# Kernel optimization log

Hardware: AMD Instinct MI355X
Metric: run time of the kernel (lower is better)

## Reference

```python
import jax, jax.numpy as jnp
import numpy as np

NEG_SLOPE = 0.2   # LeakyReLU default negative slope (GATv2 + nn.LeakyReLU)
K_NEIGH = 16      # att_args['num_neighs']


def leaky(x):
    return jnp.where(x >= 0, x, NEG_SLOPE * x)


def knn_idx(x_feat, y_feat, k):
    """Per-batch KNN of y in x (feature space). x_feat,y_feat: [B,M,C] -> [B,M,k] local idx into x."""
    d = (jnp.sum(y_feat * y_feat, -1, keepdims=True)
         - 2.0 * jnp.einsum('bmc,bnc->bmn', y_feat, x_feat)
         + jnp.sum(x_feat * x_feat, -1)[:, None, :])   # [B,M,M]
    _, idx = jax.lax.top_k(-d, k)
    return idx


def gatv2_bipartite(x_last, x_past, nbr, Wl, Wr, att_w):
    """Faithful GATv2Conv((last, past), edge_index) with flow='target_to_source',
    heads H, concat=False (mean over heads), bias=False, no self loops.
    x_j = lin_l(x[0]=last) gathered at knn neighbor (col) indices,
    x_i = lin_r(x[1]=past) at query (row) indices; each query has exactly K edges."""
    N, C = x_last.shape
    H = att_w.shape[0]
    xl = (x_last @ Wl).reshape(N, H, C)          # [N,H,C]
    xr = (x_past @ Wr).reshape(N, H, C)          # [N,H,C]
    xlj = xl[nbr]                                 # [N,K,H,C] gathered source msgs
    e = jnp.einsum('nkhc,hc->nkh', leaky(xlj + xr[:, None]), att_w)  # [N,K,H]
    a = jax.nn.softmax(e, axis=1)                 # softmax over each target's K edges
    out = jnp.einsum('nkh,nkhc->nhc', a, xlj)     # [N,H,C]
    return out.mean(axis=1)                       # concat=False -> head mean, [N,C]


def reference(pc_encoded_seq, W1, b1, W2, b2, Wl, Wr, att_w, batch_size, m_points):
    T, N, C = pc_encoded_seq.shape
    B, M = batch_size, m_points
    G = W2.shape[1]
    # node_level_proj (Linear-LeakyReLU-Linear-LeakyReLU) + global_mean_pool per frame
    h = leaky(leaky(pc_encoded_seq @ W1 + b1) @ W2 + b2)      # [T,N,G]
    global_fea = h.reshape(T, B, M, G).mean(axis=2)            # [T,B,G]
    # frame-level ScaledDotProductAttention: q = last frame, k=v = past frames
    q = global_fea[-1][:, None, :]                             # [B,1,G]
    kv = jnp.transpose(global_fea[:-1], (1, 0, 2))             # [B,T-1,G]
    score = jnp.einsum('bqg,btg->bqt', q, kv) / jnp.sqrt(jnp.asarray(G, jnp.float32))
    attn = jax.nn.softmax(score, axis=-1)                      # [B,1,T-1]
    last = pc_encoded_seq[-1]                                  # [N,C]
    lastb = last.reshape(B, M, C)
    offs = (jnp.arange(B) * M)[:, None, None]
    res = []
    for i in range(T - 1):   # small fixed frame count
        past = pc_encoded_seq[i]
        nbr = knn_idx(past.reshape(B, M, C), lastb, K_NEIGH) + offs  # global idx
        out = gatv2_bipartite(last, past, nbr.reshape(N, K_NEIGH), Wl, Wr, att_w)
        res.append(out.reshape(B, M, C))
    res = jnp.stack(res, axis=1)                               # [B,T-1,M,C]
    fw = attn[:, 0, :, None, None]                             # [B,T-1,1,1]
    weighted = jnp.sum(res * fw, axis=1)                       # [B,M,C]
    tm_out = jnp.concatenate([last, weighted.reshape(N, C)], axis=-1)  # [N,2C]
    return tm_out


def setup_inputs() -> dict:
    key = jax.random.key(0)
    ks = jax.random.split(key, 8)
    T, B, M, C, G, H = 5, 4, 4096, 128, 1024, 4
    N = B * M
    s = lambda fan: 1.0 / np.sqrt(fan)
    return {
        'pc_encoded_seq': jax.random.normal(ks[0], (T, N, C), jnp.float32),
        'W1': jax.random.normal(ks[1], (C, 128), jnp.float32) * s(C),
        'b1': jnp.zeros((128,), jnp.float32),
        'W2': jax.random.normal(ks[2], (128, G), jnp.float32) * s(128),
        'b2': jnp.zeros((G,), jnp.float32),
        'Wl': jax.random.normal(ks[3], (C, H * C), jnp.float32) * s(C),
        'Wr': jax.random.normal(ks[4], (C, H * C), jnp.float32) * s(C),
        'att_w': jax.random.normal(ks[5], (H, C), jnp.float32) * s(C),
        'batch_size': B,
        'm_points': M,
    }
```

## Files before the change

kernel.cpp:

```cpp
#include <hip/hip_runtime.h>
#include <hip/hip_bf16.h>
#include <hip/hip_fp16.h>


typedef __bf16 v8bf __attribute__((ext_vector_type(8)));
typedef float  v4f  __attribute__((ext_vector_type(4)));

__device__ __forceinline__ float lrelu(float x) { return fmaxf(x, 0.2f * x); }

__device__ __forceinline__ unsigned short f2bf(float x) {
  __hip_bfloat16 h = __float2bfloat16(x);
  return __builtin_bit_cast(unsigned short, h);
}
__device__ __forceinline__ float bf2f(unsigned short u) {
  unsigned int t = ((unsigned int)u) << 16;
  return __builtin_bit_cast(float, t);
}

#define GLOAD_LDS16(gp, lp)                                                   \
  __builtin_amdgcn_global_load_lds(                                           \
      (const __attribute__((address_space(1))) void*)(gp),                    \
      (__attribute__((address_space(3))) void*)(lp), 16, 0, 0)

#define RBAR() do { __builtin_amdgcn_s_barrier(); asm volatile("" ::: "memory"); } while (0)
#define LBAR() do { asm volatile("s_waitcnt lgkmcnt(0)" ::: "memory");         \
                    __builtin_amdgcn_s_barrier();                              \
                    asm volatile("" ::: "memory"); } while (0)

template<int EP>
__global__ __launch_bounds__(256, 2)
void nt_mfma(const unsigned short* __restrict__ A, const unsigned short* __restrict__ B,
             const float* __restrict__ aux, void* __restrict__ outv, int K, int ldc)
{
  __shared__ __align__(16) unsigned short smem[3 * 8192];
  const int tid = threadIdx.x;
  const int l = tid & 63;
  const int w = tid >> 6;
  const int wm = w & 1, wn = w >> 1;
  const int m0 = blockIdx.y << 7, n0 = blockIdx.x << 7;
  const int fr = l & 15, quad = l >> 4;
  const int kt = K >> 5;
  const int xq4 = quad ^ ((fr >> 1) & 3);

  const int r0 = tid >> 2;
  const int sw = (tid & 3) ^ ((tid >> 3) & 3);
  const unsigned short* Aa = A + (size_t)(m0 + r0) * K + sw * 8;
  const unsigned short* Ab = Aa + (size_t)64 * K;
  const unsigned short* Ba = B + (size_t)(n0 + r0) * K + sw * 8;
  const unsigned short* Bb = Ba + (size_t)64 * K;

  auto stage = [&](int bi, int ks) {
    unsigned short* As = smem + bi * 8192;
    unsigned short* Bs = As + 4096;
    GLOAD_LDS16(Aa + ks * 32, As + tid * 8);
    GLOAD_LDS16(Ab + ks * 32, As + (tid + 256) * 8);
    GLOAD_LDS16(Ba + ks * 32, Bs + tid * 8);
    GLOAD_LDS16(Bb + ks * 32, Bs + (tid + 256) * 8);
  };

  v4f acc[4][4];
#pragma unroll
  for (int i = 0; i < 4; ++i)
#pragma unroll
    for (int j = 0; j < 4; ++j) acc[i][j] = (v4f){0.f, 0.f, 0.f, 0.f};

  stage(0, 0);
  if (kt > 1) stage(1, 1);
  int cur = 0, pend = (kt > 1) ? 2 : 1, sn = 2;

  for (int ks = 0; ks < kt; ++ks) {
    if (pend == 2) asm volatile("s_waitcnt vmcnt(4)" ::: "memory");
    else           asm volatile("s_waitcnt vmcnt(0)" ::: "memory");
    RBAR();
    int nb = cur + 2; if (nb >= 3) nb -= 3;
    if (sn < kt) { stage(nb, sn); ++sn; } else { --pend; }
    const unsigned short* As = smem + cur * 8192;
    const unsigned short* Bs = As + 4096;
    v8bf af[4], bfr[4];
#pragma unroll
    for (int i = 0; i < 4; ++i)
      af[i] = *(const v8bf*)(As + (wm * 64 + i * 16 + fr) * 32 + xq4 * 8);
#pragma unroll
    for (int j = 0; j < 4; ++j)
      bfr[j] = *(const v8bf*)(Bs + (wn * 64 + j * 16 + fr) * 32 + xq4 * 8);
#pragma unroll
    for (int i = 0; i < 4; ++i)
#pragma unroll
      for (int j = 0; j < 4; ++j)
        acc[i][j] = __builtin_amdgcn_mfma_f32_16x16x32_bf16(af[i], bfr[j], acc[i][j], 0, 0, 0);
    __builtin_amdgcn_sched_barrier(0);
    if (++cur == 3) cur = 0;
  }

  if (EP == 1) {
    unsigned short* O = (unsigned short*)outv;
#pragma unroll
    for (int j = 0; j < 4; ++j) {
      int col = n0 + wn * 64 + j * 16 + fr;
      float bias = aux[col];
#pragma unroll
      for (int i = 0; i < 4; ++i) {
        int row = m0 + wm * 64 + i * 16 + quad * 4;
#pragma unroll
        for (int r = 0; r < 4; ++r)
          O[(size_t)(row + r) * ldc + col] = f2bf(lrelu(acc[i][j][r] + bias));
      }
    }
  } else if (EP == 2) {
    __syncthreads();
    float* red = (float*)smem;
#pragma unroll
    for (int j = 0; j < 4; ++j) {
      int lcol = wn * 64 + j * 16 + fr;
      float bias = aux[n0 + lcol];
      float s = 0.f;
#pragma unroll
      for (int i = 0; i < 4; ++i)
#pragma unroll
        for (int r = 0; r < 4; ++r) s += lrelu(acc[i][j][r] + bias);
      s += __shfl_xor(s, 16);
      s += __shfl_xor(s, 32);
      if (quad == 0) red[w * 128 + lcol] = s;
    }
    __syncthreads();
    if (tid < 128) {
      float s = (tid < 64) ? red[0 * 128 + tid] + red[1 * 128 + tid]
                           : red[2 * 128 + tid] + red[3 * 128 + tid];
      atomicAdd((float*)outv + ((m0 >> 12) << 10) + n0 + tid, s * (1.0f / 4096.0f));
    }
  } else {
    __half* O = (__half*)outv;
#pragma unroll
    for (int j = 0; j < 4; ++j) {
      int col = n0 + wn * 64 + j * 16 + fr;
#pragma unroll
      for (int i = 0; i < 4; ++i) {
        int row = m0 + wm * 64 + i * 16 + quad * 4;
#pragma unroll
        for (int r = 0; r < 4; ++r)
          O[(size_t)(row + r) * ldc + col] = __float2half(acc[i][j][r]);
      }
    }
  }
}

__global__ __launch_bounds__(256, 2)
void knn_fused(const unsigned short* __restrict__ ylay,
               const unsigned short* __restrict__ xlay,
               const float* __restrict__ xsq, int* __restrict__ nbrOut)
{
  __shared__ __align__(16) unsigned short smem[3 * 8192];
  __shared__ float candV[128 * 24];
  __shared__ int   candI[128 * 24];
  __shared__ float tauS[128];
  __shared__ int   cntS[128];
  __shared__ int   flagS;

  const int tid = threadIdx.x;
  const int l = tid & 63;
  const int w = tid >> 6;
  const int wm = w & 1, wn = w >> 1;
  const int pair = blockIdx.x >> 5;
  const int rb = blockIdx.x & 31;
  const int f = pair >> 2, b = pair & 3;
  const int m0 = rb << 7;
  const int fr = l & 15, quad = l >> 4;
  const int xq4 = quad ^ ((fr >> 1) & 3);

  const unsigned short* A = ylay + (size_t)b * 4096 * 384;
  const unsigned short* B = xlay + ((size_t)f * 16384 + (size_t)b * 4096) * 384;
  const float* xq = xsq + f * 16384 + b * 4096;

  const int r0 = tid >> 2;
  const int sw = (tid & 3) ^ ((tid >> 3) & 3);
  const unsigned short* Aa = A + (size_t)(m0 + r0) * 384 + sw * 8;
  const unsigned short* Ab = Aa + 64 * 384;
  const unsigned short* Brow = B + (size_t)r0 * 384 + sw * 8;

  auto stage = [&](int bi, int ct, int ks) {
    unsigned short* As = smem + bi * 8192;
    unsigned short* Bs = As + 4096;
    const unsigned short* Bt = Brow + ct * 49152 + ks * 32;
    GLOAD_LDS16(Aa + ks * 32, As + tid * 8);
    GLOAD_LDS16(Ab + ks * 32, As + (tid + 256) * 8);
    GLOAD_LDS16(Bt, Bs + tid * 8);
    GLOAD_LDS16(Bt + 64 * 384, Bs + (tid + 256) * 8);
  };

  float tv[16];
  int   ti[16];
#pragma unroll
  for (int k = 0; k < 16; ++k) { tv[k] = -3.0e38f; ti[k] = k; }
  float ownMin = -3.0e38f;
  int ownMinPos = 0;
  if (tid < 128) { tauS[tid] = -3.0e38f; cntS[tid] = 0; }
  if (tid == 0) flagS = 0;

  float tc[16];
#pragma unroll
  for (int i = 0; i < 16; ++i) tc[i] = -3.0e38f;

  stage(0, 0, 0);
  stage(1, 0, 1);
  int cur = 0, pend = 2, sct = 0, sks = 2;

  LBAR();

  for (int ct = 0; ct < 32; ++ct) {
    const int n0 = ct << 7;
    float xs[4];
#pragma unroll
    for (int j = 0; j < 4; ++j) xs[j] = xq[n0 + wn * 64 + j * 16 + fr];

    v4f acc[4][4];
#pragma unroll
    for (int i = 0; i < 4; ++i)
#pragma unroll
      for (int j = 0; j < 4; ++j) acc[i][j] = (v4f){0.f, 0.f, 0.f, 0.f};

    for (int ks = 0; ks < 12; ++ks) {
      if (pend == 2) asm volatile("s_waitcnt vmcnt(4)" ::: "memory");
      else           asm volatile("s_waitcnt vmcnt(0)" ::: "memory");
      RBAR();
      int nb = cur + 2; if (nb >= 3) nb -= 3;
      if (sct < 32) {
        stage(nb, sct, sks);
        if (++sks == 12) { sks = 0; ++sct; }
      } else { --pend; }
      const unsigned short* As = smem + cur * 8192;
      const unsigned short* Bs = As + 4096;
      v8bf af[4], bfr[4];
#pragma unroll
      for (int i = 0; i < 4; ++i)
        af[i] = *(const v8bf*)(As + (wm * 64 + i * 16 + fr) * 32 + xq4 * 8);
#pragma unroll
      for (int j = 0; j < 4; ++j)
        bfr[j] = *(const v8bf*)(Bs + (wn * 64 + j * 16 + fr) * 32 + xq4 * 8);
#pragma unroll
      for (int i = 0; i < 4; ++i)
#pragma unroll
        for (int j = 0; j < 4; ++j)
          acc[i][j] = __builtin_amdgcn_mfma_f32_16x16x32_bf16(af[i], bfr[j], acc[i][j], 0, 0, 0);
      __builtin_amdgcn_sched_barrier(0);
      if (++cur == 3) cur = 0;
    }

    unsigned long long pushed = 0ull;
    for (;;) {
#pragma unroll
      for (int i = 0; i < 4; ++i)
#pragma unroll
        for (int r = 0; r < 4; ++r) {
          const int lrow = wm * 64 + i * 16 + quad * 4 + r;
          const float tau = tc[i * 4 + r];
#pragma unroll
          for (int j = 0; j < 4; ++j) {
            const int bit = i * 16 + j * 4 + r;
            float v = 2.f * acc[i][j][r] - xs[j];
            if (v > tau && !((pushed >> bit) & 1ull)) {
              int pos = atomicAdd(&cntS[lrow], 1);
              if (pos < 24) {
                candV[lrow * 24 + pos] = v;
                candI[lrow * 24 + pos] = n0 + wn * 64 + j * 16 + fr;
                pushed |= (1ull << bit);
              }
            }
          }
        }
      LBAR();
      if (tid < 128) {
        int c = cntS[tid];
        int cc = c < 24 ? c : 24;
        for (int q = 0; q < cc; ++q) {
          float v = candV[tid * 24 + q];
          if (v > ownMin) {
            tv[ownMinPos] = v;
            ti[ownMinPos] = candI[tid * 24 + q];
            ownMin = tv[0]; ownMinPos = 0;
#pragma unroll
            for (int k = 1; k < 16; ++k)
              if (tv[k] < ownMin) { ownMin = tv[k]; ownMinPos = k; }
          }
        }
        tauS[tid] = ownMin;
        if (c > 24) flagS = 1;
        cntS[tid] = 0;
      }
      LBAR();
#pragma unroll
      for (int i = 0; i < 4; ++i)
#pragma unroll
        for (int r = 0; r < 4; ++r)
          tc[i * 4 + r] = tauS[wm * 64 + i * 16 + quad * 4 + r];
      int ov = flagS;
      LBAR();
      if (tid == 0) flagS = 0;
      if (!ov) break;
    }
  }

  if (tid < 128) {
    const int base = b * 4096;
    int* outp = nbrOut + ((size_t)(f * 16384 + b * 4096) + m0 + tid) * 16;
#pragma unroll
    for (int k = 0; k < 16; ++k) outp[k] = base + ti[k];
  }
}

__global__ __launch_bounds__(256)
void convert_inputs(const float* __restrict__ seq, unsigned short* __restrict__ seqbf,
                    unsigned short* __restrict__ ylay, unsigned short* __restrict__ xlay,
                    float* __restrict__ xsq)
{
  const int tid = threadIdx.x;
  const int row = blockIdx.x * 8 + (tid >> 5);
  const int c4 = tid & 31;
  float4 v = *(const float4*)(seq + (size_t)row * 128 + c4 * 4);
  ushort4 hi, lo;
  hi.x = f2bf(v.x); lo.x = f2bf(v.x - bf2f(hi.x));
  hi.y = f2bf(v.y); lo.y = f2bf(v.y - bf2f(hi.y));
  hi.z = f2bf(v.z); lo.z = f2bf(v.z - bf2f(hi.z));
  hi.w = f2bf(v.w); lo.w = f2bf(v.w - bf2f(hi.w));
  *(ushort4*)(seqbf + (size_t)row * 128 + c4 * 4) = hi;
  float ss = v.x * v.x + v.y * v.y + v.z * v.z + v.w * v.w;
#pragma unroll
  for (int off = 16; off; off >>= 1) ss += __shfl_xor(ss, off);
  if (row < 65536) {
    unsigned short* p = xlay + (size_t)row * 384 + c4 * 4;
    *(ushort4*)(p) = hi; *(ushort4*)(p + 128) = lo; *(ushort4*)(p + 256) = hi;
    if (c4 == 0) xsq[row] = ss;
  } else {
    unsigned short* p = ylay + (size_t)(row - 65536) * 384 + c4 * 4;
    *(ushort4*)(p) = hi; *(ushort4*)(p + 128) = hi; *(ushort4*)(p + 256) = lo;
  }
}

__global__ __launch_bounds__(256)
void convert_weights(const float* __restrict__ W1, const float* __restrict__ W2,
                     const float* __restrict__ Wl, const float* __restrict__ Wr,
                     const float* __restrict__ aw,
                     unsigned short* __restrict__ W1t, unsigned short* __restrict__ W2t,
                     unsigned short* __restrict__ Wlv, unsigned short* __restrict__ Wrv,
                     __half* __restrict__ awh)
{
  int idx = blockIdx.x * 256 + threadIdx.x;
  if (idx < 16384) {
    int n = idx >> 7, k = idx & 127;
    W1t[idx] = f2bf(W1[k * 128 + n]);
  } else if (idx < 147456) {
    int i = idx - 16384; int n = i >> 7, k = i & 127;
    W2t[i] = f2bf(W2[k * 1024 + n]);
  } else if (idx < 344064) {
    int i = idx - 147456; int n = i / 384, k = i % 384;
    int s = k >> 7, kk = k & 127;
    float wv = Wl[kk * 512 + n];
    unsigned short h = f2bf(wv);
    Wlv[i] = (s == 1) ? f2bf(wv - bf2f(h)) : h;
  } else if (idx < 540672) {
    int i = idx - 344064; int n = i / 384, k = i % 384;
    int s = k >> 7, kk = k & 127;
    float wv = Wr[kk * 512 + n];
    unsigned short h = f2bf(wv);
    Wrv[i] = (s == 2) ? f2bf(wv - bf2f(h)) : h;
  } else if (idx < 541184) {
    int i = idx - 540672;
    awh[i] = __float2half(aw[i]);
  }
}

__global__ __launch_bounds__(1024)
void temporal_attn(const float* __restrict__ gfea, float* __restrict__ attnw)
{
  const int tid = threadIdx.x;
  const int w = tid >> 6, l = tid & 63;
  const int b = w >> 2, i = w & 3;
  const float* q  = gfea + (16 + b) * 1024;
  const float* kv = gfea + (i * 4 + b) * 1024;
  float p = 0.f;
  for (int g = l; g < 1024; g += 64) p += q[g] * kv[g];
#pragma unroll
  for (int off = 32; off; off >>= 1) p += __shfl_xor(p, off);
  __shared__ float sc[16];
  if (l == 0) sc[w] = p * 0.03125f;
  __syncthreads();
  if (tid < 4) {
    float v0 = sc[tid * 4 + 0], v1 = sc[tid * 4 + 1];
    float v2 = sc[tid * 4 + 2], v3 = sc[tid * 4 + 3];
    float mm = fmaxf(fmaxf(v0, v1), fmaxf(v2, v3));
    v0 = __expf(v0 - mm); v1 = __expf(v1 - mm);
    v2 = __expf(v2 - mm); v3 = __expf(v3 - mm);
    float inv = 1.f / (v0 + v1 + v2 + v3);
    attnw[tid * 4 + 0] = v0 * inv;
    attnw[tid * 4 + 1] = v1 * inv;
    attnw[tid * 4 + 2] = v2 * inv;
    attnw[tid * 4 + 3] = v3 * inv;
  }
}

__global__ __launch_bounds__(256)
void gat6(const __half* __restrict__ xlh, const __half* __restrict__ xrh,
          const int* __restrict__ nbr, const __half* __restrict__ awh,
          const float* __restrict__ attnw, float* __restrict__ wgt4)
{
  const int tid = threadIdx.x;
  const int l = tid & 63;
  const int blk = blockIdx.x;
  const int r8 = blk & 7;
  const int b = r8 >> 1;
  const int g = ((blk >> 3) << 1) | (r8 & 1);
  const int f = g >> 10;
  const int n4 = g & 1023;
  const int qid = f * 16384 + b * 4096 + n4 * 4 + (tid >> 6);
  const int h = l >> 4, cp = l & 15;
  const float fw = attnw[b * 4 + f] * 0.25f;

  const int jl = nbr[qid * 16 + (l & 15)];
  const __half* xbase = xlh + h * 128 + cp * 8;

  const __half2* xrp = (const __half2*)(xrh + (size_t)qid * 512 + h * 128 + cp * 8);
  float2 xr0 = __half22float2(xrp[0]), xr1 = __half22float2(xrp[1]);
  float2 xr2 = __half22float2(xrp[2]), xr3 = __half22float2(xrp[3]);
  const __half2* awp = (const __half2*)(awh + h * 128 + cp * 8);
  float2 aw0 = __half22float2(awp[0]), aw1 = __half22float2(awp[1]);
  float2 aw2 = __half22float2(awp[2]), aw3 = __half22float2(awp[3]);

  float m = -3.0e38f, s = 0.f;
  float o[8];
#pragma unroll
  for (int c = 0; c < 8; ++c) o[c] = 0.f;

  for (int ch = 0; ch < 2; ++ch) {
    float4 xv[8];
#pragma unroll
    for (int k = 0; k < 8; ++k) {
      int j = __shfl(jl, ch * 8 + k);
      xv[k] = *(const float4*)(xbase + (size_t)j * 512);
    }
    float e[8];
#pragma unroll
    for (int k = 0; k < 8; ++k) {
      const __half2* hp = (const __half2*)&xv[k];
      float2 x0 = __half22float2(hp[0]), x1 = __half22float2(hp[1]);
      float2 x2 = __half22float2(hp[2]), x3 = __half22float2(hp[3]);
      float p = 0.f;
      p += lrelu(x0.x + xr0.x) * aw0.x + lrelu(x0.y + xr0.y) * aw0.y;
      p += lrelu(x1.x + xr1.x) * aw1.x + lrelu(x1.y + xr1.y) * aw1.y;
      p += lrelu(x2.x + xr2.x) * aw2.x + lrelu(x2.y + xr2.y) * aw2.y;
      p += lrelu(x3.x + xr3.x) * aw3.x + lrelu(x3.y + xr3.y) * aw3.y;
      p += __shfl_xor(p, 1);
      p += __shfl_xor(p, 2);
      p += __shfl_xor(p, 4);
      p += __shfl_xor(p, 8);
      e[k] = p;
    }
    float mc = e[0];
#pragma unroll
    for (int k = 1; k < 8; ++k) mc = fmaxf(mc, e[k]);
    float mn = fmaxf(m, mc);
    float cr = __expf(m - mn);
    s *= cr;
#pragma unroll
    for (int c = 0; c < 8; ++c) o[c] *= cr;
#pragma unroll
    for (int k = 0; k < 8; ++k) {
      float a = __expf(e[k] - mn);
      s += a;
      const __half2* hp = (const __half2*)&xv[k];
      float2 f0 = __half22float2(hp[0]);
      float2 f1 = __half22float2(hp[1]);
      float2 f2 = __half22float2(hp[2]);
      float2 f3 = __half22float2(hp[3]);
      o[0] += a * f0.x; o[1] += a * f0.y;
      o[2] += a * f1.x; o[3] += a * f1.y;
      o[4] += a * f2.x; o[5] += a * f2.y;
      o[6] += a * f3.x; o[7] += a * f3.y;
    }
    m = mn;
  }

  const float sc = fw / s;
#pragma unroll
  for (int c = 0; c < 8; ++c) {
    float t = o[c] * sc;
    t += __shfl_xor(t, 16);
    t += __shfl_xor(t, 32);
    o[c] = t;
  }
  if (l < 16) {
    float* wp = wgt4 + (size_t)qid * 128 + l * 8;
    *(float4*)(wp)     = make_float4(o[0], o[1], o[2], o[3]);
    *(float4*)(wp + 4) = make_float4(o[4], o[5], o[6], o[7]);
  }
}

__global__ __launch_bounds__(256)
void finalize2(const float* __restrict__ last, const float* __restrict__ wgt4,
               float* __restrict__ out)
{
  int idx = blockIdx.x * 256 + threadIdx.x;
  int n = idx >> 6, q = idx & 63;
  float4 v;
  if (q < 32) {
    v = *(const float4*)(last + (size_t)n * 128 + 4 * q);
  } else {
    int c = (q - 32) * 4;
    v = make_float4(0.f, 0.f, 0.f, 0.f);
#pragma unroll
    for (int f = 0; f < 4; ++f) {
      float4 t = *(const float4*)(wgt4 + ((size_t)f * 16384 + n) * 128 + c);
      v.x += t.x; v.y += t.y; v.z += t.z; v.w += t.w;
    }
  }
  *(float4*)(out + (size_t)n * 256 + 4 * q) = v;
}

extern "C" void kernel_launch(void* const* d_in, const int* in_sizes, int n_in,
                              void* d_out, int out_size, void* d_ws, size_t ws_size,
                              hipStream_t stream)
{
  (void)in_sizes; (void)n_in; (void)out_size; (void)ws_size;
  const float* seq = (const float*)d_in[0];
  const float* W1  = (const float*)d_in[1];
  const float* b1  = (const float*)d_in[2];
  const float* W2  = (const float*)d_in[3];
  const float* b2  = (const float*)d_in[4];
  const float* Wl  = (const float*)d_in[5];
  const float* Wr  = (const float*)d_in[6];
  const float* aw  = (const float*)d_in[7];
  float* out = (float*)d_out;

  float* ws = (float*)d_ws;
  __half* xrh          = (__half*)ws;
  unsigned short* seqbf = (unsigned short*)(ws + 16777216);
  unsigned short* h1bf  = (unsigned short*)(ws + 22020096);
  __half* xlh           = (__half*)(ws + 22020096);
  unsigned short* ylay  = (unsigned short*)(ws + 27262976);
  unsigned short* xlay  = (unsigned short*)(ws + 30408704);
  float* wgt4           = ws + 30408704;
  float* gfea           = ws + 42991616;
  float* attn           = gfea + 20480;
  float* xsq            = attn + 16;
  int*   nbr            = (int*)(xsq + 65536);
  unsigned short* W1t   = (unsigned short*)(nbr + 1048576);
  unsigned short* W2t   = W1t + 16384;
  unsigned short* Wlv   = W2t + 131072;
  unsigned short* Wrv   = Wlv + 196608;
  __half* awh           = (__half*)(Wrv + 196608);

  (void)hipMemsetAsync(gfea, 0, 20480 * sizeof(float), stream);

  convert_inputs<<<10240, 256, 0, stream>>>(seq, seqbf, ylay, xlay, xsq);
  convert_weights<<<2114, 256, 0, stream>>>(W1, W2, Wl, Wr, aw, W1t, W2t, Wlv, Wrv, awh);

  nt_mfma<1><<<dim3(1, 640), 256, 0, stream>>>(seqbf, W1t, b1, h1bf, 128, 128);
  nt_mfma<2><<<dim3(8, 640), 256, 0, stream>>>(h1bf, W2t, b2, gfea, 128, 0);
  temporal_attn<<<1, 1024, 0, stream>>>(gfea, attn);

  knn_fused<<<512, 256, 0, stream>>>(ylay, xlay, xsq, nbr);

  nt_mfma<3><<<dim3(4, 128), 256, 0, stream>>>(ylay, Wlv, nullptr, xlh, 384, 512);
  nt_mfma<3><<<dim3(4, 512), 256, 0, stream>>>(xlay, Wrv, nullptr, xrh, 384, 512);

  gat6<<<16384, 256, 0, stream>>>(xlh, xrh, nbr, awh, attn, wgt4);

  finalize2<<<4096, 256, 0, stream>>>(seq + (size_t)4 * 16384 * 128, wgt4, out);
}
```

Baseline: 857.3 us.

## Split KNN into bf16 coarse top-24 pass and fp32 exact rescore

The KNN kernel previously ran its distance GEMM over a 3-term bf16 split (K=384) to reach near-fp32 accuracy. It now uses a single bf16 pass (K=128) with the query tile held in registers, keeping 24 candidates per query. A new kernel rescores those 24 candidates in fp32 and picks the exact top-16. This cuts GEMM work and LDS traffic to about a third, at the cost of an extra launch and the risk that a true neighbor falls outside the bf16 top-24.

```diff
diff --git a/kernel.cpp b/kernel.cpp
--- a/kernel.cpp
+++ b/kernel.cpp
@@ -144,17 +144,19 @@
   }
 }
 
+#define CAP 24
+
 __global__ __launch_bounds__(256, 2)
-void knn_fused(const unsigned short* __restrict__ ylay,
-               const unsigned short* __restrict__ xlay,
-               const float* __restrict__ xsq, int* __restrict__ nbrOut)
-{
-  __shared__ __align__(16) unsigned short smem[3 * 8192];
-  __shared__ float candV[128 * 24];
-  __shared__ int   candI[128 * 24];
-  __shared__ float tauS[128];
-  __shared__ int   cntS[128];
-  __shared__ int   flagS;
+void knn_coarse(const unsigned short* __restrict__ seqbf,
+                const float* __restrict__ xsq, int* __restrict__ candOut)
+{
+  __shared__ __align__(16) unsigned short smem[16384];
+  __shared__ __align__(16) unsigned short bbuf[3 * 4096];
+  float* candV  = (float*)smem;
+  int*   candI  = (int*)(smem + 6144);
+  float* tauS   = (float*)(smem + 12288);
+  int*   cntS   = (int*)(smem + 12544);
+  int*   flagSp = (int*)(smem + 12800);
 
   const int tid = threadIdx.x;
   const int l = tid & 63;
@@ -167,44 +169,58 @@
   const int fr = l & 15, quad = l >> 4;
   const int xq4 = quad ^ ((fr >> 1) & 3);
 
-  const unsigned short* A = ylay + (size_t)b * 4096 * 384;
-  const unsigned short* B = xlay + ((size_t)f * 16384 + (size_t)b * 4096) * 384;
+  const unsigned short* ybase = seqbf + ((size_t)65536 + b * 4096) * 128;
+  const unsigned short* xbase = seqbf + ((size_t)(f * 16384 + b * 4096)) * 128;
   const float* xq = xsq + f * 16384 + b * 4096;
 
   const int r0 = tid >> 2;
   const int sw = (tid & 3) ^ ((tid >> 3) & 3);
-  const unsigned short* Aa = A + (size_t)(m0 + r0) * 384 + sw * 8;
-  const unsigned short* Ab = Aa + 64 * 384;
-  const unsigned short* Brow = B + (size_t)r0 * 384 + sw * 8;
-
-  auto stage = [&](int bi, int ct, int ks) {
-    unsigned short* As = smem + bi * 8192;
-    unsigned short* Bs = As + 4096;
-    const unsigned short* Bt = Brow + ct * 49152 + ks * 32;
-    GLOAD_LDS16(Aa + ks * 32, As + tid * 8);
-    GLOAD_LDS16(Ab + ks * 32, As + (tid + 256) * 8);
+  const unsigned short* Brow = xbase + (size_t)r0 * 128 + sw * 8;
+
+  auto stageB = [&](int bi, int ct, int ks) {
+    unsigned short* Bs = bbuf + bi * 4096;
+    const unsigned short* Bt = Brow + ct * 16384 + ks * 32;
     GLOAD_LDS16(Bt, Bs + tid * 8);
-    GLOAD_LDS16(Bt + 64 * 384, Bs + (tid + 256) * 8);
+    GLOAD_LDS16(Bt + 64 * 128, Bs + (tid + 256) * 8);
   };
 
-  float tv[16];
-  int   ti[16];
-#pragma unroll
-  for (int k = 0; k < 16; ++k) { tv[k] = -3.0e38f; ti[k] = k; }
+#pragma unroll
+  for (int kk = 0; kk < 4; ++kk) {
+    const unsigned short* Ag = ybase + (size_t)(m0 + r0) * 128 + kk * 32 + sw * 8;
+    GLOAD_LDS16(Ag, smem + kk * 4096 + tid * 8);
+    GLOAD_LDS16(Ag + 64 * 128, smem + kk * 4096 + (tid + 256) * 8);
+  }
+  stageB(0, 0, 0);
+  stageB(1, 0, 1);
+
+  asm volatile("s_waitcnt vmcnt(4)" ::: "memory");
+  RBAR();
+
+  v8bf afr[4][4];
+#pragma unroll
+  for (int kk = 0; kk < 4; ++kk)
+#pragma unroll
+    for (int i = 0; i < 4; ++i)
+      afr[kk][i] = *(const v8bf*)(smem + kk * 4096 + (wm * 64 + i * 16 + fr) * 32 + xq4 * 8);
+
+  LBAR();
+
+  float tv[CAP];
+  int   ti[CAP];
+#pragma unroll
+  for (int k = 0; k < CAP; ++k) { tv[k] = -3.0e38f; ti[k] = k; }
   float ownMin = -3.0e38f;
   int ownMinPos = 0;
   if (tid < 128) { tauS[tid] = -3.0e38f; cntS[tid] = 0; }
-  if (tid == 0) flagS = 0;
+  if (tid == 0) *flagSp = 0;
 
   float tc[16];
 #pragma unroll
   for (int i = 0; i < 16; ++i) tc[i] = -3.0e38f;
 
-  stage(0, 0, 0);
-  stage(1, 0, 1);
+  LBAR();
+
   int cur = 0, pend = 2, sct = 0, sks = 2;
-
-  LBAR();
 
   for (int ct = 0; ct < 32; ++ct) {
     const int n0 = ct << 7;
@@ -218,21 +234,18 @@
 #pragma unroll
       for (int j = 0; j < 4; ++j) acc[i][j] = (v4f){0.f, 0.f, 0.f, 0.f};
 
-    for (int ks = 0; ks < 12; ++ks) {
-      if (pend == 2) asm volatile("s_waitcnt vmcnt(4)" ::: "memory");
+#pragma unroll
+    for (int ks = 0; ks < 4; ++ks) {
+      if (pend == 2) asm volatile("s_waitcnt vmcnt(2)" ::: "memory");
       else           asm volatile("s_waitcnt vmcnt(0)" ::: "memory");
       RBAR();
       int nb = cur + 2; if (nb >= 3) nb -= 3;
       if (sct < 32) {
-        stage(nb, sct, sks);
-        if (++sks == 12) { sks = 0; ++sct; }
+        stageB(nb, sct, sks);
+        if (++sks == 4) { sks = 0; ++sct; }
       } else { --pend; }
-      const unsigned short* As = smem + cur * 8192;
-      const unsigned short* Bs = As + 4096;
-      v8bf af[4], bfr[4];
-#pragma unroll
-      for (int i = 0; i < 4; ++i)
-        af[i] = *(const v8bf*)(As + (wm * 64 + i * 16 + fr) * 32 + xq4 * 8);
+      const unsigned short* Bs = bbuf + cur * 4096;
+      v8bf bfr[4];
 #pragma unroll
       for (int j = 0; j < 4; ++j)
         bfr[j] = *(const v8bf*)(Bs + (wn * 64 + j * 16 + fr) * 32 + xq4 * 8);
@@ -240,7 +253,7 @@
       for (int i = 0; i < 4; ++i)
 #pragma unroll
         for (int j = 0; j < 4; ++j)
-          acc[i][j] = __builtin_amdgcn_mfma_f32_16x16x32_bf16(af[i], bfr[j], acc[i][j], 0, 0, 0);
+          acc[i][j] = __builtin_amdgcn_mfma_f32_16x16x32_bf16(afr[ks][i], bfr[j], acc[i][j], 0, 0, 0);
       __builtin_amdgcn_sched_barrier(0);
       if (++cur == 3) cur = 0;
     }
@@ -259,9 +272,9 @@
             float v = 2.f * acc[i][j][r] - xs[j];
             if (v > tau && !((pushed >> bit) & 1ull)) {
               int pos = atomicAdd(&cntS[lrow], 1);
-              if (pos < 24) {
-                candV[lrow * 24 + pos] = v;
-                candI[lrow * 24 + pos] = n0 + wn * 64 + j * 16 + fr;
+              if (pos < CAP) {
+                candV[lrow * CAP + pos] = v;
+                candI[lrow * CAP + pos] = n0 + wn * 64 + j * 16 + fr;
                 pushed |= (1ull << bit);
               }
             }
@@ -270,20 +283,20 @@
       LBAR();
       if (tid < 128) {
         int c = cntS[tid];
-        int cc = c < 24 ? c : 24;
+        int cc = c < CAP ? c : CAP;
         for (int q = 0; q < cc; ++q) {
-          float v = candV[tid * 24 + q];
+          float v = candV[tid * CAP + q];
           if (v > ownMin) {
             tv[ownMinPos] = v;
-            ti[ownMinPos] = candI[tid * 24 + q];
+            ti[ownMinPos] = candI[tid * CAP + q];
             ownMin = tv[0]; ownMinPos = 0;
 #pragma unroll
-            for (int k = 1; k < 16; ++k)
+            for (int k = 1; k < CAP; ++k)
               if (tv[k] < ownMin) { ownMin = tv[k]; ownMinPos = k; }
           }
         }
         tauS[tid] = ownMin;
-        if (c > 24) flagS = 1;
+        if (c > CAP) *flagSp = 1;
         cntS[tid] = 0;
       }
       LBAR();
@@ -292,19 +305,59 @@
 #pragma unroll
         for (int r = 0; r < 4; ++r)
           tc[i * 4 + r] = tauS[wm * 64 + i * 16 + quad * 4 + r];
-      int ov = flagS;
+      int ov = *flagSp;
       LBAR();
-      if (tid == 0) flagS = 0;
+      if (tid == 0) *flagSp = 0;
       if (!ov) break;
     }
   }
 
   if (tid < 128) {
-    const int base = b * 4096;
-    int* outp = nbrOut + ((size_t)(f * 16384 + b * 4096) + m0 + tid) * 16;
-#pragma unroll
-    for (int k = 0; k < 16; ++k) outp[k] = base + ti[k];
-  }
+    int* outp = candOut + ((size_t)(f * 16384 + b * 4096 + m0 + tid)) * CAP;
+#pragma unroll
+    for (int k = 0; k < CAP; ++k) outp[k] = ti[k];
+  }
+}
+
+__global__ __launch_bounds__(256)
+void knn_rescore(const float* __restrict__ seq, const float* __restrict__ xsq,
+                 const int* __restrict__ cand, int* __restrict__ nbrOut)
+{
+  const int tid = threadIdx.x;
+  const int l = tid & 63;
+  const int gq = blockIdx.x * 4 + (tid >> 6);
+  const int f = gq >> 14;
+  const int rem = gq & 16383;
+  const int b = rem >> 12;
+  const float2* yrow = (const float2*)(seq + ((size_t)65536 + rem) * 128);
+  const float* xslice = seq + (size_t)(f * 16384 + (b << 12)) * 128;
+  const float* xsqs = xsq + f * 16384 + (b << 12);
+
+  const float2 yv = yrow[l];
+  const int myi = cand[(size_t)gq * 24 + (l < 24 ? l : 0)];
+  float myv = -3.0e38f;
+#pragma unroll
+  for (int j = 0; j < 24; ++j) {
+    int cj = __shfl(myi, j);
+    float2 xv = ((const float2*)(xslice + (size_t)cj * 128))[l];
+    float p = yv.x * xv.x + yv.y * xv.y;
+    p += __shfl_xor(p, 1);
+    p += __shfl_xor(p, 2);
+    p += __shfl_xor(p, 4);
+    p += __shfl_xor(p, 8);
+    p += __shfl_xor(p, 16);
+    p += __shfl_xor(p, 32);
+    float v = 2.f * p - xsqs[cj];
+    if (l == j) myv = v;
+  }
+  int rank = 0;
+#pragma unroll
+  for (int j = 0; j < 24; ++j) {
+    float vj = __shfl(myv, j);
+    rank += (vj > myv || (vj == myv && j < l)) ? 1 : 0;
+  }
+  if (l < 24 && rank < 16)
+    nbrOut[(size_t)gq * 16 + rank] = (b << 12) + myi;
 }
 
 __global__ __launch_bounds__(256)
@@ -533,6 +586,7 @@
   __half* xrh          = (__half*)ws;
   unsigned short* seqbf = (unsigned short*)(ws + 16777216);
   unsigned short* h1bf  = (unsigned short*)(ws + 22020096);
+  int* cand24           = (int*)(ws + 22020096);
   __half* xlh           = (__half*)(ws + 22020096);
   unsigned short* ylay  = (unsigned short*)(ws + 27262976);
   unsigned short* xlay  = (unsigned short*)(ws + 30408704);
@@ -556,7 +610,8 @@
   nt_mfma<2><<<dim3(8, 640), 256, 0, stream>>>(h1bf, W2t, b2, gfea, 128, 0);
   temporal_attn<<<1, 1024, 0, stream>>>(gfea, attn);
 
-  knn_fused<<<512, 256, 0, stream>>>(ylay, xlay, xsq, nbr);
+  knn_coarse<<<512, 256, 0, stream>>>(seqbf, xsq, cand24);
+  knn_rescore<<<16384, 256, 0, stream>>>(seq, xsq, cand24, nbr);
 
   nt_mfma<3><<<dim3(4, 128), 256, 0, stream>>>(ylay, Wlv, nullptr, xlh, 384, 512);
   nt_mfma<3><<<dim3(4, 512), 256, 0, stream>>>(xlay, Wrv, nullptr, xrh, 384, 512);
```

Result: slower. 1.017 ms (+18.7%).
